# Kernel optimization log

Measured on AMD Instinct MI355X. Metric: run time of the kernel, lower is better.

The kernel has to match this reference:

```python
import jax, jax.numpy as jnp
import numpy as np

N = 20000          # nodes
E = 320000         # edges (avg degree 16)
FS = 1000          # feature_size (resnet feature width)
IN = 250 + FS + 250 + 85 * 3  # 1755, actual concat width


def setup_inputs() -> dict:
    key = jax.random.key(0)
    ks = jax.random.split(key, 16)
    # structured node feature matrix x: [layer_id | resnet(1000) | rel_size | rgb(3)]
    layer = jax.random.randint(ks[0], (N, 1), 1, 4).astype(jnp.float32)      # {1,2,3}
    resnet = jax.random.normal(ks[1], (N, FS), jnp.float32)
    rel = jax.random.uniform(ks[2], (N, 1), jnp.float32)                      # [0,1] -> idx 0..10
    colors = jax.random.randint(ks[3], (N, 3), 0, 256).astype(jnp.float32)
    x = jnp.concatenate([layer, resnet, rel, colors], axis=1)  # [N,1005]
    edge_index = jax.random.randint(ks[4], (2, E), 0, N)
    edge_attr = jax.random.uniform(ks[5], (E,), jnp.float32)

    def lin(k, fi, fo):
        return jax.random.normal(k, (fi, fo), jnp.float32) / np.sqrt(fi).astype(np.float32)

    return {
        "x": x,
        "edge_index": edge_index,
        "edge_attr": edge_attr,
        "layer_table": jax.random.normal(ks[6], (3, 250), jnp.float32),
        "rel_table": jax.random.normal(ks[7], (11, 250), jnp.float32),
        "color_table": jax.random.normal(ks[8], (256, 85), jnp.float32),
        "W1": lin(ks[9], IN, 512), "b1": jnp.zeros((512,), jnp.float32),
        "W2": lin(ks[10], 512, 256), "b2": jnp.zeros((256,), jnp.float32),
        "W3": lin(ks[11], 256, 64), "b3": jnp.zeros((64,), jnp.float32),
        "Wp": lin(ks[12], 64, 3), "bp": jnp.zeros((3,), jnp.float32),
    }


def _gcn_conv(h, src, dst, ew, W, b):
    # PyG GCNConv: h' = D^{-1/2} (A + I) D^{-1/2} (h W) + b, with edge weights ew
    h = h @ W
    deg = jax.ops.segment_sum(ew, dst, num_segments=N) + 1.0  # +1 for self-loop weight
    dinv = jnp.where(deg > 0.0, jax.lax.rsqrt(deg), 0.0)
    norm = dinv[src] * ew * dinv[dst]                          # [E]
    agg = jax.ops.segment_sum(h[src] * norm[:, None], dst, num_segments=N)
    agg = agg + h * (dinv * dinv)[:, None]                     # self-loop term
    return agg + b


def reference(x, edge_index, edge_attr, layer_table, rel_table, color_table,
              W1, b1, W2, b2, W3, b3, Wp, bp):
    src, dst = edge_index[0], edge_index[1]
    li = (x[:, 0] - 1.0).astype(jnp.int32)                      # layer id 0..2
    le = layer_table[li]                                        # [N,250]
    resnet = x[:, 1:FS + 1]                                     # [N,1000]
    ri = jnp.round(jnp.abs(x[:, FS + 1]) * 10.0).astype(jnp.int32)
    re = rel_table[ri]                                          # [N,250]
    ci = x[:, -3:].astype(jnp.int32)
    ce = color_table[ci].reshape(x.shape[0], -1)                # [N,255]
    h = jnp.concatenate([le, resnet, re, ce], axis=1)           # [N,1755]

    lrelu = lambda v: jax.nn.leaky_relu(v, 0.01)
    h = lrelu(_gcn_conv(h, src, dst, edge_attr, W1, b1))
    h = lrelu(_gcn_conv(h, src, dst, edge_attr, W2, b2))
    h = lrelu(_gcn_conv(h, src, dst, edge_attr, W3, b3))
    return h @ Wp + bp                                          # [N,3]
```

## Files before the change

### kernel.cpp

```cpp
#include <hip/hip_runtime.h>
#include <hip/hip_bf16.h>

#define NNODES 20000
#define NEDGES 320000
#define XW 1005
#define MP 20096

typedef __attribute__((ext_vector_type(8))) short short8;
typedef __attribute__((ext_vector_type(4))) float f32x4;
typedef __attribute__((ext_vector_type(4))) unsigned short u16x4;

typedef const __attribute__((address_space(1))) unsigned int gas_u32;
typedef __attribute__((address_space(3))) unsigned int las_u32;

__device__ inline void ld16(const unsigned short* g, unsigned short* l) {
    __builtin_amdgcn_global_load_lds((gas_u32*)g, (las_u32*)l, 16, 0, 0);
}

__device__ inline void split1(float v, unsigned short& h, unsigned short& l) {
    unsigned u = __float_as_uint(v);
    h = (unsigned short)(u >> 16);
    float hf = __uint_as_float(u & 0xffff0000u);
    l = (unsigned short)(__float_as_uint(v - hf) >> 16);
}

#define PB_EDGE  1250
#define PB_IDX   1329
#define PB_A1    21329
#define PB_BT1   21841
#define PB_BT2   21969
#define PB_BT3   21985
#define PB_TAB   23549

__device__ inline void bt_split_body(int g, const float* __restrict__ W, int ldw,
                                     int koff, int K, int Kp, int Ncols,
                                     unsigned short* __restrict__ Bh,
                                     unsigned short* __restrict__ Bl) {
    int kp4 = Kp >> 2;
    if (g >= Ncols * kp4) return;
    int n = g / kp4, c4 = (g % kp4) << 2;
    u16x4 h, l;
#pragma unroll
    for (int i = 0; i < 4; ++i) {
        int k = c4 + i;
        float v = (k < K) ? W[(size_t)(koff + k) * ldw + n] : 0.0f;
        unsigned short hh, ll;
        split1(v, hh, ll);
        h[i] = (short)hh; l[i] = (short)ll;
    }
    *(u16x4*)&Bh[(size_t)n * Kp + c4] = h;
    *(u16x4*)&Bl[(size_t)n * Kp + c4] = l;
}

__global__ __launch_bounds__(256) void prep_kernel(
    const float* __restrict__ x, const int* __restrict__ ei, const float* __restrict__ ea,
    const float* __restrict__ layer_table, const float* __restrict__ rel_table,
    const float* __restrict__ color_table,
    const float* __restrict__ W1, const float* __restrict__ W2, const float* __restrict__ W3,
    float* __restrict__ deg, int* __restrict__ counts, int* __restrict__ idx8,
    unsigned short* __restrict__ A1h, unsigned short* __restrict__ A1l,
    unsigned short* __restrict__ Bt1h, unsigned short* __restrict__ Bt1l,
    unsigned short* __restrict__ Bt2h, unsigned short* __restrict__ Bt2l,
    unsigned short* __restrict__ Bt3h, unsigned short* __restrict__ Bt3l,
    float* __restrict__ T) {
    const int b = blockIdx.x;
    const int t = threadIdx.x;
    if (b < PB_EDGE) {
        int e = b * 256 + t;
        if (e >= NEDGES) return;
        int dst = ei[NEDGES + e];
        atomicAdd(&deg[dst], ea[e]);
        atomicAdd(&counts[dst], 1);
    } else if (b < PB_IDX) {
        int i = (b - PB_EDGE) * 256 + t;
        if (i >= NNODES) return;
        const float* r = x + (size_t)i * XW;
        idx8[i * 8 + 0] = (int)(r[0] - 1.0f);
        idx8[i * 8 + 1] = (int)rintf(fabsf(r[1001]) * 10.0f);
        idx8[i * 8 + 2] = (int)r[1002];
        idx8[i * 8 + 3] = (int)r[1003];
        idx8[i * 8 + 4] = (int)r[1004];
    } else if (b < PB_A1) {
        int row = b - PB_IDX;
        int c4 = t << 2;
        const float* xp = x + (size_t)row * XW + 1 + c4;
        u16x4 h, l;
#pragma unroll
        for (int i = 0; i < 4; ++i) {
            float v = (c4 + i < 1000) ? xp[i] : 0.0f;
            unsigned short hh, ll;
            split1(v, hh, ll);
            h[i] = (short)hh; l[i] = (short)ll;
        }
        *(u16x4*)&A1h[(size_t)row * 1024 + c4] = h;
        *(u16x4*)&A1l[(size_t)row * 1024 + c4] = l;
    } else if (b < PB_BT1) {
        bt_split_body((b - PB_A1) * 256 + t, W1, 512, 250, 1000, 1024, 512, Bt1h, Bt1l);
    } else if (b < PB_BT2) {
        bt_split_body((b - PB_BT1) * 256 + t, W2, 256, 0, 512, 512, 256, Bt2h, Bt2l);
    } else if (b < PB_BT3) {
        bt_split_body((b - PB_BT2) * 256 + t, W3, 64, 0, 256, 256, 64, Bt3h, Bt3l);
    } else {
        int g = (b - PB_BT3) * 256 + t;
        if (g >= 782 * 512) return;
        int row = g >> 9, col = g & 511;
        float acc = 0.0f;
        if (row < 3) {
            for (int k = 0; k < 250; ++k)
                acc += layer_table[row * 250 + k] * W1[(size_t)k * 512 + col];
        } else if (row < 14) {
            int r = row - 3;
            for (int k = 0; k < 250; ++k)
                acc += rel_table[r * 250 + k] * W1[(size_t)(1250 + k) * 512 + col];
        } else {
            int r = row - 14;
            int j = r >> 8, v = r & 255;
            int base = 1500 + 85 * j;
            for (int k = 0; k < 85; ++k)
                acc += color_table[v * 85 + k] * W1[(size_t)(base + k) * 512 + col];
        }
        T[(size_t)row * 512 + col] = acc;
    }
}


__global__ __launch_bounds__(1024) void scan_p1_kernel(const int* __restrict__ counts,
                                                       int* __restrict__ bsum,
                                                       const float* __restrict__ deg,
                                                       float* __restrict__ dinv, int n) {
    int b = blockIdx.x;
    if (b < 20) {
        __shared__ int ws[16];
        int t = threadIdx.x, lane = t & 63, wid = t >> 6;
        int i = b * 1024 + t;
        int v = (i < n) ? counts[i] : 0;
#pragma unroll
        for (int d = 32; d; d >>= 1) v += __shfl_down(v, d, 64);
        if (lane == 0) ws[wid] = v;
        __syncthreads();
        if (wid == 0) {
            int s = (lane < 16) ? ws[lane] : 0;
#pragma unroll
            for (int d = 8; d; d >>= 1) s += __shfl_down(s, d, 64);
            if (lane == 0) bsum[b] = s;
        }
    } else {
        int i = (b - 20) * 1024 + threadIdx.x;
        if (i < n) { float d = deg[i] + 1.0f; dinv[i] = 1.0f / sqrtf(d); }
    }
}

__global__ void scan_p2_kernel(const int* __restrict__ bsum, int* __restrict__ boffs,
                               int* __restrict__ offs, int n, int nb) {
    int lane = threadIdx.x;
    int v = (lane < nb) ? bsum[lane] : 0;
    int xv = v;
#pragma unroll
    for (int d = 1; d < 64; d <<= 1) {
        int u = __shfl_up(xv, d, 64);
        if (lane >= d) xv += u;
    }
    if (lane < nb) boffs[lane] = xv - v;
    if (lane == nb - 1) offs[n] = xv;
}

__global__ __launch_bounds__(1024) void scan_p3_kernel(const int* __restrict__ counts,
                                                       const int* __restrict__ boffs,
                                                       int* __restrict__ offs, int n) {
    __shared__ int wsum[16], wpre[16];
    int t = threadIdx.x, lane = t & 63, wid = t >> 6;
    int i = blockIdx.x * 1024 + t;
    int v = (i < n) ? counts[i] : 0;
    int xv = v;
#pragma unroll
    for (int d = 1; d < 64; d <<= 1) {
        int u = __shfl_up(xv, d, 64);
        if (lane >= d) xv += u;
    }
    if (lane == 63) wsum[wid] = xv;
    __syncthreads();
    if (wid == 0) {
        int s = (lane < 16) ? wsum[lane] : 0;
#pragma unroll
        for (int d = 1; d < 16; d <<= 1) {
            int u = __shfl_up(s, d, 64);
            if (lane >= d) s += u;
        }
        if (lane < 16) wpre[lane] = s;
    }
    __syncthreads();
    int prefix = boffs[blockIdx.x] + (wid > 0 ? wpre[wid - 1] : 0);
    if (i < n) offs[i] = prefix + xv - v;
}

__global__ void scatter_kernel(const int* __restrict__ ei, const float* __restrict__ ea,
                               const float* __restrict__ dinv, const int* __restrict__ offs,
                               int* __restrict__ cursor, int* __restrict__ csr_src,
                               float* __restrict__ csr_norm, int E) {
    int e = blockIdx.x * 256 + threadIdx.x;
    if (e >= E) return;
    int src = ei[e];
    int dst = ei[E + e];
    int slot = offs[dst] + atomicAdd(&cursor[dst], 1);
    csr_src[slot] = src;
    csr_norm[slot] = dinv[src] * ea[e] * dinv[dst];
}


template <int BN, int NCB, bool EMB>
__global__ __launch_bounds__(256, 4) void gemm_split_kernel(
    const unsigned short* __restrict__ Ah, const unsigned short* __restrict__ Al, int Kp,
    const unsigned short* __restrict__ Bh, const unsigned short* __restrict__ Bl,
    float* __restrict__ C, int ldc, int M,
    const float* __restrict__ T, const int* __restrict__ idx8) {
    constexpr int NT = BN / 32;
    constexpr int BJ = BN / 64;
    __shared__ __align__(16) unsigned short sAh[64 * 32];
    __shared__ __align__(16) unsigned short sAl[64 * 32];
    __shared__ __align__(16) unsigned short sBh[BN * 32];
    __shared__ __align__(16) unsigned short sBl[BN * 32];

    const int t = threadIdx.x;
    const int lane = t & 63;
    const int w = t >> 6;
    const int wr = w >> 1, wc = w & 1;
    const int l15 = lane & 15, quad = lane >> 4;

    const int total = gridDim.x;
    const int per = total >> 3;
    const int bid = blockIdx.x;
    const int tile = (bid < (per << 3)) ? ((bid & 7) * per + (bid >> 3)) : bid;
    const int row0 = (tile / NCB) * 64;
    const int col0 = (tile % NCB) * BN;

    const int si_r = lane >> 2;
    const int si_s = lane & 3;
    const int schunk = si_s ^ ((si_r >> 1) & 3);
    const int sw = (quad ^ ((l15 >> 1) & 3)) * 8;

    const unsigned short* gAh; const unsigned short* gAl;
    unsigned short* dAh; unsigned short* dAl;
    {
        int ra = w * 16 + si_r;
        size_t e = (size_t)(row0 + ra) * Kp + schunk * 8;
        gAh = Ah + e; gAl = Al + e;
        dAh = &sAh[(w * 16) * 32];
        dAl = &sAl[(w * 16) * 32];
    }
    const unsigned short* gBh[BJ]; const unsigned short* gBl[BJ];
    unsigned short* dBh[BJ]; unsigned short* dBl[BJ];
#pragma unroll
    for (int j = 0; j < BJ; ++j) {
        int rb = w * (BN / 4) + j * 16 + si_r;
        size_t e = (size_t)(col0 + rb) * Kp + schunk * 8;
        gBh[j] = Bh + e; gBl[j] = Bl + e;
        dBh[j] = &sBh[(w * (BN / 4) + j * 16) * 32];
        dBl[j] = &sBl[(w * (BN / 4) + j * 16) * 32];
    }

    f32x4 acc[2][NT];
#pragma unroll
    for (int i = 0; i < 2; ++i)
#pragma unroll
        for (int j = 0; j < NT; ++j)
            acc[i][j] = (f32x4){0.f, 0.f, 0.f, 0.f};

    for (int kb = 0; kb < Kp; kb += 32) {
        ld16(gAh + kb, dAh);
        ld16(gAl + kb, dAl);
#pragma unroll
        for (int j = 0; j < BJ; ++j) {
            ld16(gBh[j] + kb, dBh[j]);
            ld16(gBl[j] + kb, dBl[j]);
        }
        __syncthreads();

        short8 fah[2], fal[2], fbh[NT], fbl[NT];
#pragma unroll
        for (int mt = 0; mt < 2; ++mt) {
            int off = (wr * 32 + mt * 16 + l15) * 32 + sw;
            fah[mt] = *(const short8*)&sAh[off];
            fal[mt] = *(const short8*)&sAl[off];
        }
#pragma unroll
        for (int nt = 0; nt < NT; ++nt) {
            int off = (wc * (BN / 2) + nt * 16 + l15) * 32 + sw;
            fbh[nt] = *(const short8*)&sBh[off];
            fbl[nt] = *(const short8*)&sBl[off];
        }
#pragma unroll
        for (int mt = 0; mt < 2; ++mt)
#pragma unroll
            for (int nt = 0; nt < NT; ++nt)
                acc[mt][nt] = __builtin_amdgcn_mfma_f32_16x16x32_bf16(fah[mt], fbh[nt], acc[mt][nt], 0, 0, 0);
#pragma unroll
        for (int mt = 0; mt < 2; ++mt)
#pragma unroll
            for (int nt = 0; nt < NT; ++nt)
                acc[mt][nt] = __builtin_amdgcn_mfma_f32_16x16x32_bf16(fah[mt], fbl[nt], acc[mt][nt], 0, 0, 0);
#pragma unroll
        for (int mt = 0; mt < 2; ++mt)
#pragma unroll
            for (int nt = 0; nt < NT; ++nt)
                acc[mt][nt] = __builtin_amdgcn_mfma_f32_16x16x32_bf16(fal[mt], fbh[nt], acc[mt][nt], 0, 0, 0);
        __syncthreads();
    }

#pragma unroll
    for (int mt = 0; mt < 2; ++mt)
#pragma unroll
        for (int r = 0; r < 4; ++r) {
            int row = row0 + wr * 32 + mt * 16 + quad * 4 + r;
            if (row >= M) continue;
            if (EMB) {
                const int* ix = idx8 + row * 8;
                const float* t0 = T + (size_t)ix[0] * 512;
                const float* t1 = T + (size_t)(3 + ix[1]) * 512;
                const float* t2 = T + (size_t)(14 + ix[2]) * 512;
                const float* t3 = T + (size_t)(270 + ix[3]) * 512;
                const float* t4 = T + (size_t)(526 + ix[4]) * 512;
#pragma unroll
                for (int nt = 0; nt < NT; ++nt) {
                    int col = col0 + wc * (BN / 2) + nt * 16 + l15;
                    float e = t0[col] + t1[col] + t2[col] + t3[col] + t4[col];
                    C[(size_t)row * ldc + col] = acc[mt][nt][r] + e;
                }
            } else {
#pragma unroll
                for (int nt = 0; nt < NT; ++nt) {
                    int col = col0 + wc * (BN / 2) + nt * 16 + l15;
                    C[(size_t)row * ldc + col] = acc[mt][nt][r];
                }
            }
        }
}


template <int F, int CW, bool SPLIT>
__global__ __launch_bounds__(256) void agg_cols_kernel(
    const float* __restrict__ H, const float* __restrict__ dinv,
    const int* __restrict__ offs, const int* __restrict__ csr_src,
    const float* __restrict__ csr_norm, const float* __restrict__ bias,
    float* __restrict__ outf, unsigned short* __restrict__ Hh,
    unsigned short* __restrict__ Hl, int n_nodes) {
    constexpr int LPN = CW / 4;
    constexpr int NPB = 256 / LPN;
    constexpr int NCH = F / CW;
    constexpr int ECAP = 2048;
    __shared__ int   se[ECAP];
    __shared__ float sn[ECAP];

    const int chunk = blockIdx.x & (NCH - 1);
    const int nb    = blockIdx.x / NCH;
    const int n0 = nb * NPB;
    const int n1 = min(n0 + NPB, n_nodes);
    if (n0 >= n_nodes) return;

    const int estart = offs[n0];
    const int eend   = offs[n1];
    const int ecnt   = eend - estart;
    const bool inlds = (ecnt <= ECAP);
    if (inlds) {
        for (int i = threadIdx.x; i < ecnt; i += 256) {
            se[i] = csr_src[estart + i];
            sn[i] = csr_norm[estart + i];
        }
    }
    __syncthreads();

    const int n = n0 + threadIdx.x / LPN;
    if (n >= n_nodes) return;
    const int lane = threadIdx.x % LPN;
    const int c = chunk * CW + lane * 4;

    float di = dinv[n];
    float s = di * di;
    float4 h = *(const float4*)(H + (size_t)n * F + c);
    float4 acc = make_float4(h.x * s, h.y * s, h.z * s, h.w * s);
    int e0 = offs[n], e1 = offs[n + 1];
    if (inlds) {
        for (int e = e0 - estart; e < e1 - estart; ++e) {
            int src = se[e];
            float w = sn[e];
            float4 v = *(const float4*)(H + (size_t)src * F + c);
            acc.x += v.x * w; acc.y += v.y * w; acc.z += v.z * w; acc.w += v.w * w;
        }
    } else {
        for (int e = e0; e < e1; ++e) {
            int src = csr_src[e];
            float w = csr_norm[e];
            float4 v = *(const float4*)(H + (size_t)src * F + c);
            acc.x += v.x * w; acc.y += v.y * w; acc.z += v.z * w; acc.w += v.w * w;
        }
    }
    float4 b = *(const float4*)(bias + c);
    acc.x += b.x; acc.y += b.y; acc.z += b.z; acc.w += b.w;
    acc.x = acc.x > 0.f ? acc.x : 0.01f * acc.x;
    acc.y = acc.y > 0.f ? acc.y : 0.01f * acc.y;
    acc.z = acc.z > 0.f ? acc.z : 0.01f * acc.z;
    acc.w = acc.w > 0.f ? acc.w : 0.01f * acc.w;
    if (SPLIT) {
        u16x4 hh, ll;
        unsigned short a, bb;
        split1(acc.x, a, bb); hh[0] = (short)a; ll[0] = (short)bb;
        split1(acc.y, a, bb); hh[1] = (short)a; ll[1] = (short)bb;
        split1(acc.z, a, bb); hh[2] = (short)a; ll[2] = (short)bb;
        split1(acc.w, a, bb); hh[3] = (short)a; ll[3] = (short)bb;
        *(u16x4*)(Hh + (size_t)n * F + c) = hh;
        *(u16x4*)(Hl + (size_t)n * F + c) = ll;
    } else {
        *(float4*)(outf + (size_t)n * F + c) = acc;
    }
}


__global__ void proj_kernel(const float* __restrict__ H, const float* __restrict__ Wp,
                            const float* __restrict__ bp, float* __restrict__ out, int n_nodes) {
    int t = blockIdx.x * 192 + threadIdx.x;
    int n = t / 3, j = t % 3;
    if (n >= n_nodes) return;
    float acc = bp[j];
    const float* h = H + (size_t)n * 64;
    for (int c = 0; c < 64; ++c) acc += h[c] * Wp[c * 3 + j];
    out[n * 3 + j] = acc;
}


static inline size_t aln(size_t v) { return (v + 255) & ~(size_t)255; }

extern "C" void kernel_launch(void* const* d_in, const int* in_sizes, int n_in,
                              void* d_out, int out_size, void* d_ws, size_t ws_size,
                              hipStream_t stream) {
    const float* x           = (const float*)d_in[0];
    const int*   edge_index  = (const int*)d_in[1];
    const float* edge_attr   = (const float*)d_in[2];
    const float* layer_table = (const float*)d_in[3];
    const float* rel_table   = (const float*)d_in[4];
    const float* color_table = (const float*)d_in[5];
    const float* W1 = (const float*)d_in[6];
    const float* b1 = (const float*)d_in[7];
    const float* W2 = (const float*)d_in[8];
    const float* b2 = (const float*)d_in[9];
    const float* W3 = (const float*)d_in[10];
    const float* b3 = (const float*)d_in[11];
    const float* Wp = (const float*)d_in[12];
    const float* bp = (const float*)d_in[13];
    float* out = (float*)d_out;

    const int N = NNODES, E = NEDGES;

    char* p = (char*)d_ws;
    float* deg      = (float*)p;
    int*   counts   = (int*)(p + (size_t)N * 4);
    int*   cursor   = (int*)(p + (size_t)N * 8);     p += aln((size_t)N * 12);
    float* dinv     = (float*)p; p += aln((size_t)N * 4);
    float* T        = (float*)p; p += aln((size_t)782 * 512 * 4);
    float* csr_norm = (float*)p; p += aln((size_t)E * 4);
    float* C        = (float*)p; p += aln((size_t)MP * 512 * 4);
    unsigned short* BIG = (unsigned short*)p; p += aln((size_t)MP * 2048 * 2);
    unsigned short* Bt1h = (unsigned short*)p; p += aln((size_t)512 * 1024 * 2);
    unsigned short* Bt1l = (unsigned short*)p; p += aln((size_t)512 * 1024 * 2);
    unsigned short* Bt2h = (unsigned short*)p; p += aln((size_t)256 * 512 * 2);
    unsigned short* Bt2l = (unsigned short*)p; p += aln((size_t)256 * 512 * 2);
    unsigned short* Bt3h = (unsigned short*)p; p += aln((size_t)64 * 256 * 2);
    unsigned short* Bt3l = (unsigned short*)p; p += aln((size_t)64 * 256 * 2);
    int*   csr_src  = (int*)p;   p += aln((size_t)E * 4);
    int*   idx8     = (int*)p;   p += aln((size_t)N * 8 * 4);
    int*   offs     = (int*)p;   p += aln((size_t)(N + 1) * 4);
    int*   bsum     = (int*)p;   p += aln((size_t)32 * 4);
    int*   boffs    = (int*)p;   p += aln((size_t)32 * 4);

    unsigned short* A1h = BIG;
    unsigned short* A1l = BIG + (size_t)MP * 1024;
    unsigned short* H2h = BIG;
    unsigned short* H2l = BIG + (size_t)MP * 512;
    unsigned short* H3h = BIG + (size_t)MP * 1024;
    unsigned short* H3l = BIG + (size_t)MP * 1024 + (size_t)MP * 256;
    float*          H4  = (float*)(BIG + (size_t)MP * 1536);

    hipMemsetAsync(deg, 0, (size_t)N * 12, stream);

    prep_kernel<<<PB_TAB, 256, 0, stream>>>(
        x, edge_index, edge_attr, layer_table, rel_table, color_table,
        W1, W2, W3, deg, counts, idx8,
        A1h, A1l, Bt1h, Bt1l, Bt2h, Bt2l, Bt3h, Bt3l, T);

    scan_p1_kernel<<<40, 1024, 0, stream>>>(counts, bsum, deg, dinv, N);
    scan_p2_kernel<<<1, 64, 0, stream>>>(bsum, boffs, offs, N, 20);
    scan_p3_kernel<<<20, 1024, 0, stream>>>(counts, boffs, offs, N);
    scatter_kernel<<<(E + 255) / 256, 256, 0, stream>>>(edge_index, edge_attr, dinv, offs,
                                                        cursor, csr_src, csr_norm, E);

    const int nrb = MP / 64;

    {
        gemm_split_kernel<128, 4, true><<<nrb * 4, 256, 0, stream>>>(
            A1h, A1l, 1024, Bt1h, Bt1l, C, 512, N, T, idx8);
        int nblocks = (N + 15) / 16;
        agg_cols_kernel<512, 64, true><<<8 * nblocks, 256, 0, stream>>>(
            C, dinv, offs, csr_src, csr_norm, b1, nullptr, H2h, H2l, N);
    }
    {
        gemm_split_kernel<128, 2, false><<<nrb * 2, 256, 0, stream>>>(
            H2h, H2l, 512, Bt2h, Bt2l, C, 256, N, nullptr, nullptr);
        int nblocks = (N + 31) / 32;
        agg_cols_kernel<256, 32, true><<<8 * nblocks, 256, 0, stream>>>(
            C, dinv, offs, csr_src, csr_norm, b2, nullptr, H3h, H3l, N);
    }
    {
        gemm_split_kernel<64, 1, false><<<nrb, 256, 0, stream>>>(
            H3h, H3l, 256, Bt3h, Bt3l, C, 64, N, nullptr, nullptr);
        int nblocks = (N + 63) / 64;
        agg_cols_kernel<64, 16, false><<<4 * nblocks, 256, 0, stream>>>(
            C, dinv, offs, csr_src, csr_norm, b3, H4, nullptr, nullptr, N);
    }
    proj_kernel<<<(N * 3 + 191) / 192, 192, 0, stream>>>(H4, Wp, bp, out, N);
}
```

Before: 455.5 us.

## Double-buffer split-bf16 GEMM LDS tiles and switch to 128x64 block tiles

The GEMM kernel now loads the next K-slice into a second LDS buffer while the current slice runs through MFMA, which removes one barrier per iteration and overlaps global loads with compute. Tiles change from 64xBN to a fixed 128x64, so each warp computes 4x2 MFMA tiles and grids are resized to match. This doubles LDS use and raises register pressure (launch bounds drop to 3 blocks per CU), and the smaller layer-3 grid gives fewer blocks.

```diff
diff --git a/kernel.cpp b/kernel.cpp
--- a/kernel.cpp
+++ b/kernel.cpp
@@ -207,18 +207,16 @@
 }
 
 
-template <int BN, int NCB, bool EMB>
-__global__ __launch_bounds__(256, 4) void gemm_split_kernel(
+template <int NCB, bool EMB>
+__global__ __launch_bounds__(256, 3) void gemm_split_kernel(
     const unsigned short* __restrict__ Ah, const unsigned short* __restrict__ Al, int Kp,
     const unsigned short* __restrict__ Bh, const unsigned short* __restrict__ Bl,
     float* __restrict__ C, int ldc, int M,
     const float* __restrict__ T, const int* __restrict__ idx8) {
-    constexpr int NT = BN / 32;
-    constexpr int BJ = BN / 64;
-    __shared__ __align__(16) unsigned short sAh[64 * 32];
-    __shared__ __align__(16) unsigned short sAl[64 * 32];
-    __shared__ __align__(16) unsigned short sBh[BN * 32];
-    __shared__ __align__(16) unsigned short sBl[BN * 32];
+    __shared__ __align__(16) unsigned short sAh[2][128 * 32];
+    __shared__ __align__(16) unsigned short sAl[2][128 * 32];
+    __shared__ __align__(16) unsigned short sBh[2][64 * 32];
+    __shared__ __align__(16) unsigned short sBl[2][64 * 32];
 
     const int t = threadIdx.x;
     const int lane = t & 63;
@@ -230,87 +228,104 @@
     const int per = total >> 3;
     const int bid = blockIdx.x;
     const int tile = (bid < (per << 3)) ? ((bid & 7) * per + (bid >> 3)) : bid;
-    const int row0 = (tile / NCB) * 64;
-    const int col0 = (tile % NCB) * BN;
+    const int row0 = (tile / NCB) * 128;
+    const int col0 = (tile % NCB) * 64;
 
     const int si_r = lane >> 2;
     const int si_s = lane & 3;
     const int schunk = si_s ^ ((si_r >> 1) & 3);
     const int sw = (quad ^ ((l15 >> 1) & 3)) * 8;
 
-    const unsigned short* gAh; const unsigned short* gAl;
-    unsigned short* dAh; unsigned short* dAl;
+    const unsigned short* gAh[2]; const unsigned short* gAl[2];
+    int aoff[2];
+#pragma unroll
+    for (int j = 0; j < 2; ++j) {
+        int ra = w * 32 + j * 16 + si_r;
+        size_t e = (size_t)(row0 + ra) * Kp + schunk * 8;
+        gAh[j] = Ah + e; gAl[j] = Al + e;
+        aoff[j] = (w * 32 + j * 16) * 32;
+    }
+    const unsigned short* gBh; const unsigned short* gBl;
+    int boff;
     {
-        int ra = w * 16 + si_r;
-        size_t e = (size_t)(row0 + ra) * Kp + schunk * 8;
-        gAh = Ah + e; gAl = Al + e;
-        dAh = &sAh[(w * 16) * 32];
-        dAl = &sAl[(w * 16) * 32];
-    }
-    const unsigned short* gBh[BJ]; const unsigned short* gBl[BJ];
-    unsigned short* dBh[BJ]; unsigned short* dBl[BJ];
-#pragma unroll
-    for (int j = 0; j < BJ; ++j) {
-        int rb = w * (BN / 4) + j * 16 + si_r;
+        int rb = w * 16 + si_r;
         size_t e = (size_t)(col0 + rb) * Kp + schunk * 8;
-        gBh[j] = Bh + e; gBl[j] = Bl + e;
-        dBh[j] = &sBh[(w * (BN / 4) + j * 16) * 32];
-        dBl[j] = &sBl[(w * (BN / 4) + j * 16) * 32];
-    }
-
-    f32x4 acc[2][NT];
-#pragma unroll
-    for (int i = 0; i < 2; ++i)
-#pragma unroll
-        for (int j = 0; j < NT; ++j)
+        gBh = Bh + e; gBl = Bl + e;
+        boff = (w * 16) * 32;
+    }
+
+    f32x4 acc[4][2];
+#pragma unroll
+    for (int i = 0; i < 4; ++i)
+#pragma unroll
+        for (int j = 0; j < 2; ++j)
             acc[i][j] = (f32x4){0.f, 0.f, 0.f, 0.f};
 
-    for (int kb = 0; kb < Kp; kb += 32) {
-        ld16(gAh + kb, dAh);
-        ld16(gAl + kb, dAl);
-#pragma unroll
-        for (int j = 0; j < BJ; ++j) {
-            ld16(gBh[j] + kb, dBh[j]);
-            ld16(gBl[j] + kb, dBl[j]);
-        }
+    const int nit = Kp / 32;
+
+#pragma unroll
+    for (int j = 0; j < 2; ++j) {
+        ld16(gAh[j], &sAh[0][aoff[j]]);
+        ld16(gAl[j], &sAl[0][aoff[j]]);
+    }
+    ld16(gBh, &sBh[0][boff]);
+    ld16(gBl, &sBl[0][boff]);
+
+    int cur = 0;
+    for (int kt = 0; kt < nit; ++kt) {
         __syncthreads();
-
-        short8 fah[2], fal[2], fbh[NT], fbl[NT];
-#pragma unroll
-        for (int mt = 0; mt < 2; ++mt) {
-            int off = (wr * 32 + mt * 16 + l15) * 32 + sw;
-            fah[mt] = *(const short8*)&sAh[off];
-            fal[mt] = *(const short8*)&sAl[off];
-        }
-#pragma unroll
-        for (int nt = 0; nt < NT; ++nt) {
-            int off = (wc * (BN / 2) + nt * 16 + l15) * 32 + sw;
-            fbh[nt] = *(const short8*)&sBh[off];
-            fbl[nt] = *(const short8*)&sBl[off];
-        }
-#pragma unroll
-        for (int mt = 0; mt < 2; ++mt)
-#pragma unroll
-            for (int nt = 0; nt < NT; ++nt)
+        if (kt + 1 < nit) {
+            const int kb = (kt + 1) * 32;
+            const int nb = cur ^ 1;
+#pragma unroll
+            for (int j = 0; j < 2; ++j) {
+                ld16(gAh[j] + kb, &sAh[nb][aoff[j]]);
+                ld16(gAl[j] + kb, &sAl[nb][aoff[j]]);
+            }
+            ld16(gBh + kb, &sBh[nb][boff]);
+            ld16(gBl + kb, &sBl[nb][boff]);
+        }
+
+        const unsigned short* bAh = sAh[cur];
+        const unsigned short* bAl = sAl[cur];
+        const unsigned short* bBh = sBh[cur];
+        const unsigned short* bBl = sBl[cur];
+        short8 fah[4], fal[4], fbh[2], fbl[2];
+#pragma unroll
+        for (int mt = 0; mt < 4; ++mt) {
+            int off = (wr * 64 + mt * 16 + l15) * 32 + sw;
+            fah[mt] = *(const short8*)&bAh[off];
+            fal[mt] = *(const short8*)&bAl[off];
+        }
+#pragma unroll
+        for (int nt = 0; nt < 2; ++nt) {
+            int off = (wc * 32 + nt * 16 + l15) * 32 + sw;
+            fbh[nt] = *(const short8*)&bBh[off];
+            fbl[nt] = *(const short8*)&bBl[off];
+        }
+#pragma unroll
+        for (int mt = 0; mt < 4; ++mt)
+#pragma unroll
+            for (int nt = 0; nt < 2; ++nt)
                 acc[mt][nt] = __builtin_amdgcn_mfma_f32_16x16x32_bf16(fah[mt], fbh[nt], acc[mt][nt], 0, 0, 0);
 #pragma unroll
-        for (int mt = 0; mt < 2; ++mt)
-#pragma unroll
-            for (int nt = 0; nt < NT; ++nt)
+        for (int mt = 0; mt < 4; ++mt)
+#pragma unroll
+            for (int nt = 0; nt < 2; ++nt)
                 acc[mt][nt] = __builtin_amdgcn_mfma_f32_16x16x32_bf16(fah[mt], fbl[nt], acc[mt][nt], 0, 0, 0);
 #pragma unroll
-        for (int mt = 0; mt < 2; ++mt)
-#pragma unroll
-            for (int nt = 0; nt < NT; ++nt)
+        for (int mt = 0; mt < 4; ++mt)
+#pragma unroll
+            for (int nt = 0; nt < 2; ++nt)
                 acc[mt][nt] = __builtin_amdgcn_mfma_f32_16x16x32_bf16(fal[mt], fbh[nt], acc[mt][nt], 0, 0, 0);
-        __syncthreads();
-    }
-
-#pragma unroll
-    for (int mt = 0; mt < 2; ++mt)
+        cur ^= 1;
+    }
+
+#pragma unroll
+    for (int mt = 0; mt < 4; ++mt)
 #pragma unroll
         for (int r = 0; r < 4; ++r) {
-            int row = row0 + wr * 32 + mt * 16 + quad * 4 + r;
+            int row = row0 + wr * 64 + mt * 16 + quad * 4 + r;
             if (row >= M) continue;
             if (EMB) {
                 const int* ix = idx8 + row * 8;
@@ -320,15 +335,15 @@
                 const float* t3 = T + (size_t)(270 + ix[3]) * 512;
                 const float* t4 = T + (size_t)(526 + ix[4]) * 512;
 #pragma unroll
-                for (int nt = 0; nt < NT; ++nt) {
-                    int col = col0 + wc * (BN / 2) + nt * 16 + l15;
+                for (int nt = 0; nt < 2; ++nt) {
+                    int col = col0 + wc * 32 + nt * 16 + l15;
                     float e = t0[col] + t1[col] + t2[col] + t3[col] + t4[col];
                     C[(size_t)row * ldc + col] = acc[mt][nt][r] + e;
                 }
             } else {
 #pragma unroll
-                for (int nt = 0; nt < NT; ++nt) {
-                    int col = col0 + wc * (BN / 2) + nt * 16 + l15;
+                for (int nt = 0; nt < 2; ++nt) {
+                    int col = col0 + wc * 32 + nt * 16 + l15;
                     C[(size_t)row * ldc + col] = acc[mt][nt][r];
                 }
             }
@@ -491,24 +506,24 @@
     scatter_kernel<<<(E + 255) / 256, 256, 0, stream>>>(edge_index, edge_attr, dinv, offs,
                                                         cursor, csr_src, csr_norm, E);
 
-    const int nrb = MP / 64;
+    const int nrb = MP / 128;
 
     {
-        gemm_split_kernel<128, 4, true><<<nrb * 4, 256, 0, stream>>>(
+        gemm_split_kernel<8, true><<<nrb * 8, 256, 0, stream>>>(
             A1h, A1l, 1024, Bt1h, Bt1l, C, 512, N, T, idx8);
         int nblocks = (N + 15) / 16;
         agg_cols_kernel<512, 64, true><<<8 * nblocks, 256, 0, stream>>>(
             C, dinv, offs, csr_src, csr_norm, b1, nullptr, H2h, H2l, N);
     }
     {
-        gemm_split_kernel<128, 2, false><<<nrb * 2, 256, 0, stream>>>(
+        gemm_split_kernel<4, false><<<nrb * 4, 256, 0, stream>>>(
             H2h, H2l, 512, Bt2h, Bt2l, C, 256, N, nullptr, nullptr);
         int nblocks = (N + 31) / 32;
         agg_cols_kernel<256, 32, true><<<8 * nblocks, 256, 0, stream>>>(
             C, dinv, offs, csr_src, csr_norm, b2, nullptr, H3h, H3l, N);
     }
     {
-        gemm_split_kernel<64, 1, false><<<nrb, 256, 0, stream>>>(
+        gemm_split_kernel<1, false><<<nrb, 256, 0, stream>>>(
             H3h, H3l, 256, Bt3h, Bt3l, C, 64, N, nullptr, nullptr);
         int nblocks = (N + 63) / 64;
         agg_cols_kernel<64, 16, false><<<4 * nblocks, 256, 0, stream>>>(
```

New measurement: 457.4 us. About the same (+0.4%).

## Enlarge GEMM row tile to 128 and prefetch next K-slab through registers

Applied to the files above, without the earlier changes.

The split-bf16 GEMM kernel now computes 128-row tiles instead of 64, so each wave holds four M sub-tiles and reuses every B fragment across more MFMAs. The direct global-to-LDS loads are replaced by register staging: the next K-slab is loaded into registers while the current slab is computed, then written to LDS at the start of the next iteration. Explicit waitcnt and barrier builtins replace __syncthreads. The trade is more registers and LDS per block, with launch bounds lowered to 3 blocks per CU, and half as many blocks in the grid.

```diff
diff --git a/kernel.cpp b/kernel.cpp
--- a/kernel.cpp
+++ b/kernel.cpp
@@ -10,12 +10,7 @@
 typedef __attribute__((ext_vector_type(4))) float f32x4;
 typedef __attribute__((ext_vector_type(4))) unsigned short u16x4;
 
-typedef const __attribute__((address_space(1))) unsigned int gas_u32;
-typedef __attribute__((address_space(3))) unsigned int las_u32;
-
-__device__ inline void ld16(const unsigned short* g, unsigned short* l) {
-    __builtin_amdgcn_global_load_lds((gas_u32*)g, (las_u32*)l, 16, 0, 0);
-}
+typedef const __attribute__((address_space(1))) short8* g8cp;
 
 __device__ inline void split1(float v, unsigned short& h, unsigned short& l) {
     unsigned u = __float_as_uint(v);
@@ -208,15 +203,15 @@
 
 
 template <int BN, int NCB, bool EMB>
-__global__ __launch_bounds__(256, 4) void gemm_split_kernel(
+__global__ __launch_bounds__(256, 3) void gemm_split_kernel(
     const unsigned short* __restrict__ Ah, const unsigned short* __restrict__ Al, int Kp,
     const unsigned short* __restrict__ Bh, const unsigned short* __restrict__ Bl,
     float* __restrict__ C, int ldc, int M,
     const float* __restrict__ T, const int* __restrict__ idx8) {
     constexpr int NT = BN / 32;
     constexpr int BJ = BN / 64;
-    __shared__ __align__(16) unsigned short sAh[64 * 32];
-    __shared__ __align__(16) unsigned short sAl[64 * 32];
+    __shared__ __align__(16) unsigned short sAh[128 * 32];
+    __shared__ __align__(16) unsigned short sAl[128 * 32];
     __shared__ __align__(16) unsigned short sBh[BN * 32];
     __shared__ __align__(16) unsigned short sBl[BN * 32];
 
@@ -230,7 +225,7 @@
     const int per = total >> 3;
     const int bid = blockIdx.x;
     const int tile = (bid < (per << 3)) ? ((bid & 7) * per + (bid >> 3)) : bid;
-    const int row0 = (tile / NCB) * 64;
+    const int row0 = (tile / NCB) * 128;
     const int col0 = (tile % NCB) * BN;
 
     const int si_r = lane >> 2;
@@ -238,47 +233,78 @@
     const int schunk = si_s ^ ((si_r >> 1) & 3);
     const int sw = (quad ^ ((l15 >> 1) & 3)) * 8;
 
-    const unsigned short* gAh; const unsigned short* gAl;
-    unsigned short* dAh; unsigned short* dAl;
-    {
-        int ra = w * 16 + si_r;
+    const unsigned short* gA[2][2];
+    int aoff[2];
+#pragma unroll
+    for (int j = 0; j < 2; ++j) {
+        int ra = w * 32 + j * 16 + si_r;
         size_t e = (size_t)(row0 + ra) * Kp + schunk * 8;
-        gAh = Ah + e; gAl = Al + e;
-        dAh = &sAh[(w * 16) * 32];
-        dAl = &sAl[(w * 16) * 32];
-    }
-    const unsigned short* gBh[BJ]; const unsigned short* gBl[BJ];
-    unsigned short* dBh[BJ]; unsigned short* dBl[BJ];
+        gA[j][0] = Ah + e; gA[j][1] = Al + e;
+        aoff[j] = (w * 32 + j * 16 + si_r) * 32 + si_s * 8;
+    }
+    const unsigned short* gB[BJ][2];
+    int boff[BJ];
 #pragma unroll
     for (int j = 0; j < BJ; ++j) {
         int rb = w * (BN / 4) + j * 16 + si_r;
         size_t e = (size_t)(col0 + rb) * Kp + schunk * 8;
-        gBh[j] = Bh + e; gBl[j] = Bl + e;
-        dBh[j] = &sBh[(w * (BN / 4) + j * 16) * 32];
-        dBl[j] = &sBl[(w * (BN / 4) + j * 16) * 32];
-    }
-
-    f32x4 acc[2][NT];
-#pragma unroll
-    for (int i = 0; i < 2; ++i)
+        gB[j][0] = Bh + e; gB[j][1] = Bl + e;
+        boff[j] = (w * (BN / 4) + j * 16 + si_r) * 32 + si_s * 8;
+    }
+
+    f32x4 acc[4][NT];
+#pragma unroll
+    for (int i = 0; i < 4; ++i)
 #pragma unroll
         for (int j = 0; j < NT; ++j)
             acc[i][j] = (f32x4){0.f, 0.f, 0.f, 0.f};
 
-    for (int kb = 0; kb < Kp; kb += 32) {
-        ld16(gAh + kb, dAh);
-        ld16(gAl + kb, dAl);
+    const int nit = Kp / 32;
+
+    short8 pA[2][2], pB[BJ][2];
+#pragma unroll
+    for (int j = 0; j < 2; ++j) {
+        pA[j][0] = *(g8cp)(const void*)(gA[j][0]);
+        pA[j][1] = *(g8cp)(const void*)(gA[j][1]);
+    }
+#pragma unroll
+    for (int j = 0; j < BJ; ++j) {
+        pB[j][0] = *(g8cp)(const void*)(gB[j][0]);
+        pB[j][1] = *(g8cp)(const void*)(gB[j][1]);
+    }
+
+    for (int kt = 0; kt < nit; ++kt) {
+#pragma unroll
+        for (int j = 0; j < 2; ++j) {
+            *(short8*)&sAh[aoff[j]] = pA[j][0];
+            *(short8*)&sAl[aoff[j]] = pA[j][1];
+        }
 #pragma unroll
         for (int j = 0; j < BJ; ++j) {
-            ld16(gBh[j] + kb, dBh[j]);
-            ld16(gBl[j] + kb, dBl[j]);
-        }
-        __syncthreads();
-
-        short8 fah[2], fal[2], fbh[NT], fbl[NT];
-#pragma unroll
-        for (int mt = 0; mt < 2; ++mt) {
-            int off = (wr * 32 + mt * 16 + l15) * 32 + sw;
+            *(short8*)&sBh[boff[j]] = pB[j][0];
+            *(short8*)&sBl[boff[j]] = pB[j][1];
+        }
+        if (kt + 1 < nit) {
+            const int kb = (kt + 1) * 32;
+#pragma unroll
+            for (int j = 0; j < 2; ++j) {
+                pA[j][0] = *(g8cp)(const void*)(gA[j][0] + kb);
+                pA[j][1] = *(g8cp)(const void*)(gA[j][1] + kb);
+            }
+#pragma unroll
+            for (int j = 0; j < BJ; ++j) {
+                pB[j][0] = *(g8cp)(const void*)(gB[j][0] + kb);
+                pB[j][1] = *(g8cp)(const void*)(gB[j][1] + kb);
+            }
+        }
+        __builtin_amdgcn_s_waitcnt(0xC07F);
+        __builtin_amdgcn_s_barrier();
+        __builtin_amdgcn_sched_barrier(0);
+
+        short8 fah[4], fal[4], fbh[NT], fbl[NT];
+#pragma unroll
+        for (int mt = 0; mt < 4; ++mt) {
+            int off = (wr * 64 + mt * 16 + l15) * 32 + sw;
             fah[mt] = *(const short8*)&sAh[off];
             fal[mt] = *(const short8*)&sAl[off];
         }
@@ -289,28 +315,28 @@
             fbl[nt] = *(const short8*)&sBl[off];
         }
 #pragma unroll
-        for (int mt = 0; mt < 2; ++mt)
+        for (int mt = 0; mt < 4; ++mt)
 #pragma unroll
             for (int nt = 0; nt < NT; ++nt)
                 acc[mt][nt] = __builtin_amdgcn_mfma_f32_16x16x32_bf16(fah[mt], fbh[nt], acc[mt][nt], 0, 0, 0);
 #pragma unroll
-        for (int mt = 0; mt < 2; ++mt)
+        for (int mt = 0; mt < 4; ++mt)
 #pragma unroll
             for (int nt = 0; nt < NT; ++nt)
                 acc[mt][nt] = __builtin_amdgcn_mfma_f32_16x16x32_bf16(fah[mt], fbl[nt], acc[mt][nt], 0, 0, 0);
 #pragma unroll
-        for (int mt = 0; mt < 2; ++mt)
+        for (int mt = 0; mt < 4; ++mt)
 #pragma unroll
             for (int nt = 0; nt < NT; ++nt)
                 acc[mt][nt] = __builtin_amdgcn_mfma_f32_16x16x32_bf16(fal[mt], fbh[nt], acc[mt][nt], 0, 0, 0);
-        __syncthreads();
-    }
-
-#pragma unroll
-    for (int mt = 0; mt < 2; ++mt)
+        if (kt + 1 < nit) __builtin_amdgcn_s_barrier();
+    }
+
+#pragma unroll
+    for (int mt = 0; mt < 4; ++mt)
 #pragma unroll
         for (int r = 0; r < 4; ++r) {
-            int row = row0 + wr * 32 + mt * 16 + quad * 4 + r;
+            int row = row0 + wr * 64 + mt * 16 + quad * 4 + r;
             if (row >= M) continue;
             if (EMB) {
                 const int* ix = idx8 + row * 8;
@@ -491,7 +517,7 @@
     scatter_kernel<<<(E + 255) / 256, 256, 0, stream>>>(edge_index, edge_attr, dinv, offs,
                                                         cursor, csr_src, csr_norm, E);
 
-    const int nrb = MP / 64;
+    const int nrb = MP / 128;
 
     {
         gemm_split_kernel<128, 4, true><<<nrb * 4, 256, 0, stream>>>(
```

New measurement: 447.7 us. About the same (-1.7%).
